# Optimization experiments

Measured on AMD Instinct MI355X. Metric: run time of the kernel, lower is better.

Reference implementation:

```python
import jax, jax.numpy as jnp
import numpy as np

KS = 3
K2 = KS * KS
PAD = 1


def conv2d(x, w, b=None, stride=1, pad=0):
    out = jax.lax.conv_general_dilated(
        x, w, (stride, stride), [(pad, pad), (pad, pad)],
        dimension_numbers=("NCHW", "OIHW", "NCHW"))
    if b is not None:
        out = out + b[None, :, None, None]
    return out


def setup_inputs() -> dict:
    key = jax.random.key(0)
    ks = jax.random.split(key, 11)
    B, C, H, W = 4, 64, 128, 128
    s = 0.05  # weight scale keeps offsets in a sane range
    return {
        "x":      jax.random.normal(ks[0], (B, C, H, W), jnp.float32),
        "ref":    jax.random.normal(ks[1], (B, C, H, W), jnp.float32),
        "w_cd":   jax.random.normal(ks[2], (C, 2 * C, 1, 1), jnp.float32) * s,
        "b_cd":   jax.random.normal(ks[3], (C,), jnp.float32) * s,
        "w_p":    jax.random.normal(ks[4], (2 * K2, C, 3, 3), jnp.float32) * s,
        "b_p":    jax.random.normal(ks[5], (2 * K2,), jnp.float32) * s,
        "w_m":    jax.random.normal(ks[6], (K2, C, 3, 3), jnp.float32) * s,
        "b_m":    jax.random.normal(ks[7], (K2,), jnp.float32) * s,
        "w_c":    jax.random.normal(ks[8], (K2 * C, C, 3, 3), jnp.float32) * s,
        "b_c":    jax.random.normal(ks[9], (K2 * C,), jnp.float32) * s,
        "w_conv": jax.random.normal(ks[10], (C, C, 3, 3), jnp.float32) * s,
    }


def _deform_forward(x, ref, w_cd, b_cd, w_p, b_p, w_m, b_m, w_c, b_c, w_conv):
    B, C, H, W = x.shape
    dt = x.dtype

    # offset / modulation / color nets on fused input
    fused = conv2d(jnp.concatenate([x, ref], axis=1), w_cd, b_cd)          # [B,C,H,W]
    off = conv2d(fused, w_p, b_p, pad=1)                                    # [B,2K2,H,W]
    mod = jax.nn.sigmoid(conv2d(fused, w_m, b_m, pad=1))                    # [B,K2,H,W]
    col = jnp.tanh(conv2d(fused, w_c, b_c, pad=1))                          # [B,K2*C,H,W]

    # zero-pad input; sampling grid carries the +padding shift (arange starts at 1)
    xp = jnp.pad(x, ((0, 0), (0, 0), (PAD, PAD), (PAD, PAD)))
    Hp, Wp = H + 2 * PAD, W + 2 * PAD

    gx = jnp.broadcast_to(jnp.arange(1, H + 1, dtype=dt)[:, None], (H, W))
    gy = jnp.broadcast_to(jnp.arange(1, W + 1, dtype=dt)[None, :], (H, W))
    r = (KS - 1) // 2
    cx, cy = jnp.meshgrid(jnp.arange(-r, r + 1, dtype=dt),
                          jnp.arange(-r, r + 1, dtype=dt), indexing="ij")
    px = gx[None, None] + off[:, :K2] + cx.ravel()[None, :, None, None]     # [B,K2,H,W]
    py = gy[None, None] + off[:, K2:] + cy.ravel()[None, :, None, None]

    # integer neighbors (detached, like torch .detach().floor())
    fx = jax.lax.stop_gradient(jnp.floor(px))
    fy = jax.lax.stop_gradient(jnp.floor(py))
    q_ltx = jnp.clip(fx, 0, Hp - 1); q_lty = jnp.clip(fy, 0, Wp - 1)
    q_rbx = jnp.clip(fx + 1, 0, Hp - 1); q_rby = jnp.clip(fy + 1, 0, Wp - 1)

    # clamped sampling locations for weights
    sx = jnp.clip(px, 0, Hp - 1)
    sy = jnp.clip(py, 0, Wp - 1)
    g_lt = (1 + (q_ltx - sx)) * (1 + (q_lty - sy))
    g_rb = (1 - (q_rbx - sx)) * (1 - (q_rby - sy))
    g_lb = (1 + (q_ltx - sx)) * (1 - (q_rby - sy))
    g_rt = (1 - (q_rbx - sx)) * (1 + (q_lty - sy))

    xf = xp.reshape(B, C, Hp * Wp)

    def gather(qx, qy):
        idx = (qx.astype(jnp.int32) * Wp + qy.astype(jnp.int32)).reshape(B, -1)
        out = jax.vmap(lambda m, i: m[:, i])(xf, idx)                       # [B,C,K2*H*W]
        return out.reshape(B, C, K2, H, W)

    pos = (g_lt[:, None] * gather(q_ltx, q_lty)
           + g_rb[:, None] * gather(q_rbx, q_rby)
           + g_lb[:, None] * gather(q_ltx, q_rby)
           + g_rt[:, None] * gather(q_rbx, q_lty))                          # [B,C,K2,H,W]

    inp = col.reshape(B, C, K2, H, W) + pos                                 # color deform
    inp = inp * mod[:, None]                                                # modulation

    # [B,C,kx,ky,H,W] -> [B,C,H,kx,W,ky] -> [B,C,H*ks,W*ks]
    io = inp.reshape(B, C, KS, KS, H, W).transpose(0, 1, 4, 2, 5, 3)
    io = io.reshape(B, C, H * KS, W * KS)
    return conv2d(io, w_conv, None, stride=KS)                              # [B,outc,H,W]


def reference(x, ref, w_cd, b_cd, w_p, b_p, w_m, b_m, w_c, b_c, w_conv):
    return _deform_forward(x, ref, w_cd, b_cd, w_p, b_p, w_m, b_m, w_c, b_c, w_conv)
```

## Files before the change

### kernel.cpp

```cpp
#include <hip/hip_runtime.h>
#include <hip/hip_bf16.h>
#include <math.h>

typedef short s16x8 __attribute__((ext_vector_type(8)));
typedef float f32x4 __attribute__((ext_vector_type(4)));

__device__ inline ushort f2bf(float f) {
  unsigned u = __float_as_uint(f);
  u = (u + 0x7FFF + ((u >> 16) & 1)) >> 16;
  return (ushort)u;
}
__device__ inline float bf2f(ushort u) {
  return __uint_as_float(((unsigned)u) << 16);
}
__device__ inline unsigned pkbf(float a, float b) {
  __hip_bfloat162 h = __float22bfloat162_rn(make_float2(a, b));
  return *(unsigned*)&h;
}
__device__ inline float fast_tanh(float v) {
  float e = __builtin_amdgcn_exp2f(v * 2.8853900817779268f);
  return 1.f - 2.f * __builtin_amdgcn_rcpf(e + 1.f);
}
__device__ inline float fast_sigmoid(float v) {
  float e = __builtin_amdgcn_exp2f(v * -1.4426950408889634f);
  return __builtin_amdgcn_rcpf(1.f + e);
}

__global__ __launch_bounds__(256) void k_fused(
    const float* __restrict__ x, const float* __restrict__ ref,
    const float* __restrict__ wcd, const float* __restrict__ bcd,
    const float* __restrict__ wp, const float* __restrict__ bp,
    const float* __restrict__ wm, const float* __restrict__ bm,
    const float* __restrict__ wc, const float* __restrict__ bc,
    const float* __restrict__ wconv,
    ushort* __restrict__ fusedt, ushort* __restrict__ xtb,
    ushort* __restrict__ Wpk, float* __restrict__ Bc, ushort* __restrict__ W2pk) {
  __shared__ float sxf[64][68];
  __shared__ __align__(16) ushort xt_lds[64 * 128];
  __shared__ float sb[64];

  if (blockIdx.x >= 1024) {
    int i = (blockIdx.x - 1024) * 256 + threadIdx.x;
    if (i < 368640) {
      int e = i & 7, lane = (i >> 3) & 63, mi = (i >> 9) & 3, ocq = (i >> 11) & 1;
      int hi = i >> 12;
      int ks = hi % 18, og = hi / 18;
      int g = og * 128 + ocq * 64 + mi * 16 + (lane & 15);
      int ci = ((ks & 1) << 5) + ((lane >> 4) << 3) + e;
      int kk = ks >> 1;
      int col = ci * 9 + kk;
      float v = 0.f;
      if (g < 18)       v = wp[g * 576 + col];
      else if (g < 27)  v = wm[(g - 18) * 576 + col];
      else if (g >= 64) {
        int j = g - 64;
        int cc = (j & 63) * 9 + (j >> 6);
        v = wc[cc * 576 + col];
      }
      Wpk[i] = f2bf(v);
    }
    if (i < 36864) {
      int e = i & 7, lane = (i >> 3) & 63, mi = (i >> 9) & 3, ks = i >> 11;
      int o = mi * 16 + (lane & 15);
      int p = (ks << 5) + ((lane >> 4) << 3) + e;
      int kk2 = p >> 6, c = p & 63;
      W2pk[i] = f2bf(wconv[o * 576 + c * 9 + kk2]);
    }
    if (i < 640) {
      float bv = 0.f;
      if (i < 18)       bv = bp[i];
      else if (i < 27)  bv = bm[i - 18];
      else if (i >= 64) {
        int j = i - 64;
        bv = bc[(j & 63) * 9 + (j >> 6)];
      }
      Bc[i] = bv;
    }
    return;
  }

  const int t = threadIdx.x;
  const int b = blockIdx.x >> 8, hw0 = (blockIdx.x & 255) << 6;
  if (t < 64) sb[t] = bcd[t];

  #pragma unroll
  for (int rep = 0; rep < 4; rep++) {
    int idx = t + (rep << 8);
    int ci = idx >> 4, p4 = (idx & 15) << 2;
    float4 v = *(const float4*)(x + ((size_t)((b << 6) + ci) << 14) + hw0 + p4);
    *(float4*)&sxf[ci][p4] = v;
  }
  __syncthreads();

  #pragma unroll
  for (int rep = 0; rep < 2; rep++) {
    int idx = t + (rep << 8);
    int px = idx >> 3, g = idx & 7;
    const int e0 = g << 3;
    uint4 ow;
    ow.x = pkbf(sxf[e0 + 0][px], sxf[e0 + 1][px]);
    ow.y = pkbf(sxf[e0 + 2][px], sxf[e0 + 3][px]);
    ow.z = pkbf(sxf[e0 + 4][px], sxf[e0 + 5][px]);
    ow.w = pkbf(sxf[e0 + 6][px], sxf[e0 + 7][px]);
    *(uint4*)(xt_lds + px * 128 + (((g + px) & 15) << 3)) = ow;
    *(uint4*)(xtb + (((size_t)b << 14) + hw0 + px) * 64 + (g << 3)) = ow;
  }
  __syncthreads();

  #pragma unroll
  for (int rep = 0; rep < 4; rep++) {
    int idx = t + (rep << 8);
    int ci = idx >> 4, p4 = (idx & 15) << 2;
    float4 v = *(const float4*)(ref + ((size_t)((b << 6) + ci) << 14) + hw0 + p4);
    *(float4*)&sxf[ci][p4] = v;
  }
  __syncthreads();

  #pragma unroll
  for (int rep = 0; rep < 2; rep++) {
    int idx = t + (rep << 8);
    int px = idx >> 3, g = (idx & 7) + 8;
    const int e0 = (g & 7) << 3;
    uint4 ow;
    ow.x = pkbf(sxf[e0 + 0][px], sxf[e0 + 1][px]);
    ow.y = pkbf(sxf[e0 + 2][px], sxf[e0 + 3][px]);
    ow.z = pkbf(sxf[e0 + 4][px], sxf[e0 + 5][px]);
    ow.w = pkbf(sxf[e0 + 6][px], sxf[e0 + 7][px]);
    *(uint4*)(xt_lds + px * 128 + (((g + px) & 15) << 3)) = ow;
  }
  __syncthreads();

  const int lane = t & 63, wv4 = t >> 6;
  const int ocl = lane & 15, kb = lane >> 4;
  const int ocr = (wv4 << 4) + ocl;
  f32x4 acc[4];
  #pragma unroll
  for (int ni = 0; ni < 4; ni++) acc[ni] = (f32x4){0.f, 0.f, 0.f, 0.f};
  #pragma unroll
  for (int s = 0; s < 4; s++) {
    const int gA = (s << 2) + kb;
    const float4* wr4 = (const float4*)(wcd + ocr * 128 + (gA << 3));
    float4 wa = wr4[0], wb2 = wr4[1];
    unsigned aw[4];
    aw[0] = pkbf(wa.x, wa.y);   aw[1] = pkbf(wa.z, wa.w);
    aw[2] = pkbf(wb2.x, wb2.y); aw[3] = pkbf(wb2.z, wb2.w);
    s16x8 af = *(const s16x8*)aw;
    #pragma unroll
    for (int ni = 0; ni < 4; ni++) {
      const int px = (ni << 4) + ocl;
      s16x8 bf8 = *(const s16x8*)(xt_lds + px * 128 + (((gA + px) & 15) << 3));
      acc[ni] = __builtin_amdgcn_mfma_f32_16x16x32_bf16(af, bf8, acc[ni], 0, 0, 0);
    }
  }
  const float4 b4 = *(const float4*)&sb[(wv4 << 4) + (kb << 2)];
  #pragma unroll
  for (int ni = 0; ni < 4; ni++) {
    const int px = (ni << 4) + ocl;
    uint2 o;
    o.x = pkbf(acc[ni][0] + b4.x, acc[ni][1] + b4.y);
    o.y = pkbf(acc[ni][2] + b4.z, acc[ni][3] + b4.w);
    *(uint2*)(fusedt + (((size_t)(b << 14) + hw0 + px) << 6) + (wv4 << 4) + (kb << 2)) = o;
  }
}

__global__ __launch_bounds__(256) void k_all(
    const ushort* __restrict__ Wpk, const ushort* __restrict__ fusedt,
    const float* __restrict__ Bc, const ushort* __restrict__ xtb,
    const ushort* __restrict__ W2pk, float* __restrict__ out) {
  __shared__ __align__(16) ushort sF[3 * 66 * 64];
  __shared__ __align__(16) ushort colT[64 * 64];
  __shared__ float homT[64 * 27];
  const int t = threadIdx.x;
  const int lane = t & 63, wv = t >> 6;
  const int rowid = blockIdx.x;
  const int b = rowid >> 8;
  const int rem = rowid & 255;
  const int h = rem >> 1, hf = rem & 1;
  const int w0 = hf << 6;
  const int hw0 = (h << 7) + w0;

  for (int idx = t; idx < 1584; idx += 256) {
    int p = idx >> 3, j = idx & 7;
    int row = p / 66, w1 = p - row * 66;
    int gh = h + row - 1, gw = w0 + w1 - 1;
    uint4 v = make_uint4(0u, 0u, 0u, 0u);
    if (gh >= 0 && gh < 128 && (unsigned)gw < 128u)
      v = *(const uint4*)(fusedt + ((size_t)((b << 14) + (gh << 7) + gw) << 6) + j * 8);
    int slot = (j + w1) & 7;
    *(uint4*)(sF + (p << 6) + slot * 8) = v;
  }
  __syncthreads();

  const int pxq = wv & 1, rowq = wv >> 1;
  const int nif = lane & 15, kb = lane >> 4, quad = lane >> 4;

  if (rowq == 0) {
    f32x4 acc[2][2];
    #pragma unroll
    for (int mi = 0; mi < 2; mi++)
      #pragma unroll
      for (int ni = 0; ni < 2; ni++) acc[mi][ni] = (f32x4){0.f, 0.f, 0.f, 0.f};
    __builtin_amdgcn_s_setprio(1);
    #pragma unroll 2
    for (int ks = 0; ks < 18; ks++) {
      const int kk = ks >> 1, half = ks & 1;
      const int dr = kk / 3, dc = kk - dr * 3;
      const ushort* wp8 = Wpk + ((size_t)(ks << 12)) + (lane << 3);
      s16x8 af[2], bfr[2];
      #pragma unroll
      for (int mi = 0; mi < 2; mi++)
        af[mi] = *(const s16x8*)(wp8 + (mi << 9));
      const int gci = half * 4 + kb;
      #pragma unroll
      for (int ni = 0; ni < 2; ni++) {
        int r = (pxq << 5) + ni * 16 + nif;
        int w1 = r + dc;
        int slot = (gci + w1) & 7;
        bfr[ni] = *(const s16x8*)(sF + ((dr * 66 + w1) << 6) + slot * 8);
      }
      #pragma unroll
      for (int mi = 0; mi < 2; mi++)
        #pragma unroll
        for (int ni = 0; ni < 2; ni++)
          acc[mi][ni] = __builtin_amdgcn_mfma_f32_16x16x32_bf16(af[mi], bfr[ni], acc[mi][ni], 0, 0, 0);
    }
    __builtin_amdgcn_s_setprio(0);
    #pragma unroll
    for (int mi = 0; mi < 2; mi++) {
      #pragma unroll
      for (int ni = 0; ni < 2; ni++) {
        int px = (pxq << 5) + ni * 16 + nif;
        #pragma unroll
        for (int r = 0; r < 4; r++) {
          int g = mi * 16 + (quad << 2) + r;
          float v = acc[mi][ni][r] + Bc[g];
          if (g < 18)       homT[px * 27 + g] = v;
          else if (g < 27)  homT[px * 27 + g] = fast_sigmoid(v);
        }
      }
    }
  }

  const int cq = t >> 6, pxl = t & 63, c0 = cq << 4;
  const int ww = w0 + pxl;
  const ushort* xb = xtb + ((size_t)b << 20);

  f32x4 aco[2][2];
  #pragma unroll
  for (int mi = 0; mi < 2; mi++)
    #pragma unroll
    for (int ni = 0; ni < 2; ni++) aco[mi][ni] = (f32x4){0.f, 0.f, 0.f, 0.f};

  #pragma unroll 1
  for (int k = 0; k < 9; k++) {
    const int q = 1 + k, og = q >> 1, ocq = q & 1;
    f32x4 acc[2][2];
    #pragma unroll
    for (int mi = 0; mi < 2; mi++)
      #pragma unroll
      for (int ni = 0; ni < 2; ni++) acc[mi][ni] = (f32x4){0.f, 0.f, 0.f, 0.f};
    __builtin_amdgcn_s_setprio(1);
    #pragma unroll 2
    for (int ks = 0; ks < 18; ks++) {
      const int kk = ks >> 1, half = ks & 1;
      const int dr = kk / 3, dc = kk - dr * 3;
      const ushort* wp8 = Wpk + ((size_t)((((og * 18 + ks) << 1) + ocq) << 11)) + (lane << 3);
      s16x8 af[2], bfr[2];
      #pragma unroll
      for (int mi = 0; mi < 2; mi++)
        af[mi] = *(const s16x8*)(wp8 + (((rowq << 1) + mi) << 9));
      const int gci = half * 4 + kb;
      #pragma unroll
      for (int ni = 0; ni < 2; ni++) {
        int r = (pxq << 5) + ni * 16 + nif;
        int w1 = r + dc;
        int slot = (gci + w1) & 7;
        bfr[ni] = *(const s16x8*)(sF + ((dr * 66 + w1) << 6) + slot * 8);
      }
      #pragma unroll
      for (int mi = 0; mi < 2; mi++)
        #pragma unroll
        for (int ni = 0; ni < 2; ni++)
          acc[mi][ni] = __builtin_amdgcn_mfma_f32_16x16x32_bf16(af[mi], bfr[ni], acc[mi][ni], 0, 0, 0);
    }
    __builtin_amdgcn_s_setprio(0);
    __syncthreads();

    #pragma unroll
    for (int mi = 0; mi < 2; mi++) {
      #pragma unroll
      for (int ni = 0; ni < 2; ni++) {
        int px = (pxq << 5) + ni * 16 + nif;
        int c = (rowq << 5) + mi * 16 + (quad << 2);
        float4 b4 = *(const float4*)(Bc + 64 + (k << 6) + c);
        ushort v4[4];
        v4[0] = f2bf(fast_tanh(acc[mi][ni][0] + b4.x));
        v4[1] = f2bf(fast_tanh(acc[mi][ni][1] + b4.y));
        v4[2] = f2bf(fast_tanh(acc[mi][ni][2] + b4.z));
        v4[3] = f2bf(fast_tanh(acc[mi][ni][3] + b4.w));
        int slot = ((c >> 3) + px) & 7;
        *(uint2*)(colT + (px << 6) + slot * 8 + (c & 7)) = *(uint2*)v4;
      }
    }
    __syncthreads();

    {
      float ox = homT[pxl * 27 + k];
      float oy = homT[pxl * 27 + 9 + k];
      float mk = homT[pxl * 27 + 18 + k];
      float px_ = (float)(h + k / 3) + ox;
      float py_ = (float)(ww + k % 3) + oy;
      float fx = floorf(px_), fy = floorf(py_);
      float qltx = fminf(fmaxf(fx, 0.f), 129.f);
      float qlty = fminf(fmaxf(fy, 0.f), 129.f);
      float qrbx = fminf(fmaxf(fx + 1.f, 0.f), 129.f);
      float qrby = fminf(fmaxf(fy + 1.f, 0.f), 129.f);
      float sx = fminf(fmaxf(px_, 0.f), 129.f);
      float sy = fminf(fmaxf(py_, 0.f), 129.f);
      float ax = 1.f + qltx - sx, bx = 1.f - qrbx + sx;
      float ay = 1.f + qlty - sy, by = 1.f - qrby + sy;
      int iltx = (int)qltx, ilty = (int)qlty, irbx = (int)qrbx, irby = (int)qrby;
      bool vltx = (iltx >= 1) && (iltx <= 128);
      bool vlty = (ilty >= 1) && (ilty <= 128);
      bool vrbx = (irbx >= 1) && (irbx <= 128);
      bool vrby = (irby >= 1) && (irby <= 128);
      float wl[4];
      int   ofs[4];
      wl[0] = (vltx && vlty) ? ax * ay : 0.f;
      wl[1] = (vrbx && vrby) ? bx * by : 0.f;
      wl[2] = (vltx && vrby) ? ax * by : 0.f;
      wl[3] = (vrbx && vlty) ? bx * ay : 0.f;
      ofs[0] = (vltx && vlty) ? ((iltx - 1) << 7) + (ilty - 1) : 0;
      ofs[1] = (vrbx && vrby) ? ((irbx - 1) << 7) + (irby - 1) : 0;
      ofs[2] = (vltx && vrby) ? ((iltx - 1) << 7) + (irby - 1) : 0;
      ofs[3] = (vrbx && vlty) ? ((irbx - 1) << 7) + (ilty - 1) : 0;

      float pos[16];
      #pragma unroll
      for (int j = 0; j < 16; j++) pos[j] = 0.f;
      #pragma unroll
      for (int corner = 0; corner < 4; corner++) {
        const ushort* p = xb + ((size_t)ofs[corner] << 6) + c0;
        float wgt = wl[corner];
        ushort tmp[16];
        *(uint4*)(tmp)     = *(const uint4*)(p);
        *(uint4*)(tmp + 8) = *(const uint4*)(p + 8);
        #pragma unroll
        for (int j = 0; j < 16; j++) pos[j] += wgt * bf2f(tmp[j]);
      }
      #pragma unroll
      for (int q2 = 0; q2 < 2; q2++) {
        int chunk = (cq << 1) + q2;
        int slot = (chunk + pxl) & 7;
        ushort* cp = colT + (pxl << 6) + slot * 8;
        ushort ct[8];
        *(uint4*)ct = *(const uint4*)cp;
        #pragma unroll
        for (int j = 0; j < 8; j++)
          ct[j] = f2bf((bf2f(ct[j]) + pos[q2 * 8 + j]) * mk);
        *(uint4*)cp = *(uint4*)ct;
      }
    }
    __syncthreads();

    __builtin_amdgcn_s_setprio(1);
    #pragma unroll
    for (int khalf = 0; khalf < 2; khalf++) {
      int ks2 = (k << 1) + khalf;
      s16x8 af[2], bfr[2];
      #pragma unroll
      for (int mi = 0; mi < 2; mi++)
        af[mi] = *(const s16x8*)(W2pk + ((((ks2 << 2) + (rowq << 1) + mi) << 6) + lane) * 8);
      const int g0 = (khalf << 2) + kb;
      #pragma unroll
      for (int ni = 0; ni < 2; ni++) {
        int r = (pxq << 5) + ni * 16 + nif;
        int slot = (g0 + r) & 7;
        bfr[ni] = *(const s16x8*)(colT + (r << 6) + slot * 8);
      }
      #pragma unroll
      for (int mi = 0; mi < 2; mi++)
        #pragma unroll
        for (int ni = 0; ni < 2; ni++)
          aco[mi][ni] = __builtin_amdgcn_mfma_f32_16x16x32_bf16(af[mi], bfr[ni], aco[mi][ni], 0, 0, 0);
    }
    __builtin_amdgcn_s_setprio(0);
  }

  #pragma unroll
  for (int mi = 0; mi < 2; mi++) {
    #pragma unroll
    for (int ni = 0; ni < 2; ni++) {
      int hwp = hw0 + (pxq << 5) + ni * 16 + nif;
      #pragma unroll
      for (int r = 0; r < 4; r++) {
        int o = (rowq << 5) + mi * 16 + (quad << 2) + r;
        out[(((size_t)b * 64 + o) << 14) + hwp] = aco[mi][ni][r];
      }
    }
  }
}

extern "C" void kernel_launch(void* const* d_in, const int* in_sizes, int n_in,
                              void* d_out, int out_size, void* d_ws, size_t ws_size,
                              hipStream_t stream) {
  const float* x     = (const float*)d_in[0];
  const float* ref   = (const float*)d_in[1];
  const float* wcd   = (const float*)d_in[2];
  const float* bcd   = (const float*)d_in[3];
  const float* wp    = (const float*)d_in[4];
  const float* bp    = (const float*)d_in[5];
  const float* wm    = (const float*)d_in[6];
  const float* bm    = (const float*)d_in[7];
  const float* wc    = (const float*)d_in[8];
  const float* bc    = (const float*)d_in[9];
  const float* wconv = (const float*)d_in[10];
  float* out = (float*)d_out;

  char* w8 = (char*)d_ws;
  ushort* Wpk     = (ushort*)(w8 + 0);
  float*  Bc      = (float*)(w8 + 737280);
  ushort* W2pk    = (ushort*)(w8 + 739840);
  ushort* fusedt  = (ushort*)(w8 + 813568);
  ushort* xtb     = (ushort*)(w8 + 9202176);

  k_fused <<<2464, 256, 0, stream>>>(x, ref, wcd, bcd, wp, bp, wm, bm, wc, bc, wconv,
                                     fusedt, xtb, Wpk, Bc, W2pk);
  k_all   <<<1024, 256, 0, stream>>>(Wpk, fusedt, Bc, xtb, W2pk, out);
}
```

Baseline: 198.2 us.

## Load NCHW input directly into transposed bf16 LDS and fold weight packing into conv blocks

The first kernel no longer stages x and ref through an fp32 shared tile with four barriers. Each thread now reads 8 channel-strided scalars per pixel, packs them to bf16 and writes them straight into the swizzled LDS tile, with a single barrier. The transposed x copy is written out from LDS afterwards. Weight and bias packing moves from 1440 dedicated extra blocks into a grid-stride tail of the 1024 conv blocks, and launch bounds request 8 blocks per CU. Dropping the fp32 tile frees LDS for occupancy, at the cost of less vectorized strided global loads.

```diff
diff --git a/kernel.cpp b/kernel.cpp
--- a/kernel.cpp
+++ b/kernel.cpp
@@ -26,7 +26,7 @@
   return __builtin_amdgcn_rcpf(1.f + e);
 }
 
-__global__ __launch_bounds__(256) void k_fused(
+__global__ __launch_bounds__(256, 8) void k_fused(
     const float* __restrict__ x, const float* __restrict__ ref,
     const float* __restrict__ wcd, const float* __restrict__ bcd,
     const float* __restrict__ wp, const float* __restrict__ bp,
@@ -35,100 +35,44 @@
     const float* __restrict__ wconv,
     ushort* __restrict__ fusedt, ushort* __restrict__ xtb,
     ushort* __restrict__ Wpk, float* __restrict__ Bc, ushort* __restrict__ W2pk) {
-  __shared__ float sxf[64][68];
   __shared__ __align__(16) ushort xt_lds[64 * 128];
   __shared__ float sb[64];
-
-  if (blockIdx.x >= 1024) {
-    int i = (blockIdx.x - 1024) * 256 + threadIdx.x;
-    if (i < 368640) {
-      int e = i & 7, lane = (i >> 3) & 63, mi = (i >> 9) & 3, ocq = (i >> 11) & 1;
-      int hi = i >> 12;
-      int ks = hi % 18, og = hi / 18;
-      int g = og * 128 + ocq * 64 + mi * 16 + (lane & 15);
-      int ci = ((ks & 1) << 5) + ((lane >> 4) << 3) + e;
-      int kk = ks >> 1;
-      int col = ci * 9 + kk;
-      float v = 0.f;
-      if (g < 18)       v = wp[g * 576 + col];
-      else if (g < 27)  v = wm[(g - 18) * 576 + col];
-      else if (g >= 64) {
-        int j = g - 64;
-        int cc = (j & 63) * 9 + (j >> 6);
-        v = wc[cc * 576 + col];
-      }
-      Wpk[i] = f2bf(v);
-    }
-    if (i < 36864) {
-      int e = i & 7, lane = (i >> 3) & 63, mi = (i >> 9) & 3, ks = i >> 11;
-      int o = mi * 16 + (lane & 15);
-      int p = (ks << 5) + ((lane >> 4) << 3) + e;
-      int kk2 = p >> 6, c = p & 63;
-      W2pk[i] = f2bf(wconv[o * 576 + c * 9 + kk2]);
-    }
-    if (i < 640) {
-      float bv = 0.f;
-      if (i < 18)       bv = bp[i];
-      else if (i < 27)  bv = bm[i - 18];
-      else if (i >= 64) {
-        int j = i - 64;
-        bv = bc[(j & 63) * 9 + (j >> 6)];
-      }
-      Bc[i] = bv;
-    }
-    return;
-  }
 
   const int t = threadIdx.x;
   const int b = blockIdx.x >> 8, hw0 = (blockIdx.x & 255) << 6;
   if (t < 64) sb[t] = bcd[t];
 
   #pragma unroll
-  for (int rep = 0; rep < 4; rep++) {
-    int idx = t + (rep << 8);
-    int ci = idx >> 4, p4 = (idx & 15) << 2;
-    float4 v = *(const float4*)(x + ((size_t)((b << 6) + ci) << 14) + hw0 + p4);
-    *(float4*)&sxf[ci][p4] = v;
+  for (int rep = 0; rep < 2; rep++) {
+    const int px = t & 63;
+    const int g = (t >> 6) + (rep << 2);
+    const float* xrow = x   + ((size_t)((b << 6) + (g << 3)) << 14) + hw0 + px;
+    const float* rrow = ref + ((size_t)((b << 6) + (g << 3)) << 14) + hw0 + px;
+    float v[8];
+    #pragma unroll
+    for (int e = 0; e < 8; e++) v[e] = xrow[(size_t)e << 14];
+    uint4 ow;
+    ow.x = pkbf(v[0], v[1]); ow.y = pkbf(v[2], v[3]);
+    ow.z = pkbf(v[4], v[5]); ow.w = pkbf(v[6], v[7]);
+    *(uint4*)(xt_lds + px * 128 + (((g + px) & 15) << 3)) = ow;
+    #pragma unroll
+    for (int e = 0; e < 8; e++) v[e] = rrow[(size_t)e << 14];
+    uint4 orf;
+    orf.x = pkbf(v[0], v[1]); orf.y = pkbf(v[2], v[3]);
+    orf.z = pkbf(v[4], v[5]); orf.w = pkbf(v[6], v[7]);
+    *(uint4*)(xt_lds + px * 128 + (((g + 8 + px) & 15) << 3)) = orf;
   }
   __syncthreads();
 
-  #pragma unroll
-  for (int rep = 0; rep < 2; rep++) {
-    int idx = t + (rep << 8);
-    int px = idx >> 3, g = idx & 7;
-    const int e0 = g << 3;
-    uint4 ow;
-    ow.x = pkbf(sxf[e0 + 0][px], sxf[e0 + 1][px]);
-    ow.y = pkbf(sxf[e0 + 2][px], sxf[e0 + 3][px]);
-    ow.z = pkbf(sxf[e0 + 4][px], sxf[e0 + 5][px]);
-    ow.w = pkbf(sxf[e0 + 6][px], sxf[e0 + 7][px]);
-    *(uint4*)(xt_lds + px * 128 + (((g + px) & 15) << 3)) = ow;
-    *(uint4*)(xtb + (((size_t)b << 14) + hw0 + px) * 64 + (g << 3)) = ow;
-  }
-  __syncthreads();
-
-  #pragma unroll
-  for (int rep = 0; rep < 4; rep++) {
-    int idx = t + (rep << 8);
-    int ci = idx >> 4, p4 = (idx & 15) << 2;
-    float4 v = *(const float4*)(ref + ((size_t)((b << 6) + ci) << 14) + hw0 + p4);
-    *(float4*)&sxf[ci][p4] = v;
-  }
-  __syncthreads();
-
-  #pragma unroll
-  for (int rep = 0; rep < 2; rep++) {
-    int idx = t + (rep << 8);
-    int px = idx >> 3, g = (idx & 7) + 8;
-    const int e0 = (g & 7) << 3;
-    uint4 ow;
-    ow.x = pkbf(sxf[e0 + 0][px], sxf[e0 + 1][px]);
-    ow.y = pkbf(sxf[e0 + 2][px], sxf[e0 + 3][px]);
-    ow.z = pkbf(sxf[e0 + 4][px], sxf[e0 + 5][px]);
-    ow.w = pkbf(sxf[e0 + 6][px], sxf[e0 + 7][px]);
-    *(uint4*)(xt_lds + px * 128 + (((g + px) & 15) << 3)) = ow;
-  }
-  __syncthreads();
+  {
+    const int px = t >> 2, j0 = (t & 3) << 1;
+    const ushort* rowp = xt_lds + px * 128;
+    uint4 c0 = *(const uint4*)(rowp + (((j0 + px) & 15) << 3));
+    uint4 c1 = *(const uint4*)(rowp + (((j0 + 1 + px) & 15) << 3));
+    ushort* dst = xtb + (((size_t)b << 14) + hw0 + px) * 64 + (j0 << 3);
+    *(uint4*)dst       = c0;
+    *(uint4*)(dst + 8) = c1;
+  }
 
   const int lane = t & 63, wv4 = t >> 6;
   const int ocl = lane & 15, kb = lane >> 4;
@@ -160,6 +104,43 @@
     o.x = pkbf(acc[ni][0] + b4.x, acc[ni][1] + b4.y);
     o.y = pkbf(acc[ni][2] + b4.z, acc[ni][3] + b4.w);
     *(uint2*)(fusedt + (((size_t)(b << 14) + hw0 + px) << 6) + (wv4 << 4) + (kb << 2)) = o;
+  }
+
+  const int gid = blockIdx.x * 256 + t;
+  for (int i = gid; i < 368640; i += 262144) {
+    int e = i & 7, lne = (i >> 3) & 63, mi = (i >> 9) & 3, ocq = (i >> 11) & 1;
+    int hi = i >> 12;
+    int ks = hi % 18, og = hi / 18;
+    int g = og * 128 + ocq * 64 + mi * 16 + (lne & 15);
+    int ci = ((ks & 1) << 5) + ((lne >> 4) << 3) + e;
+    int kk = ks >> 1;
+    int col = ci * 9 + kk;
+    float v = 0.f;
+    if (g < 18)       v = wp[g * 576 + col];
+    else if (g < 27)  v = wm[(g - 18) * 576 + col];
+    else if (g >= 64) {
+      int j = g - 64;
+      int cc = (j & 63) * 9 + (j >> 6);
+      v = wc[cc * 576 + col];
+    }
+    Wpk[i] = f2bf(v);
+  }
+  if (gid < 36864) {
+    int e = gid & 7, lne = (gid >> 3) & 63, mi = (gid >> 9) & 3, ks = gid >> 11;
+    int o = mi * 16 + (lne & 15);
+    int p = (ks << 5) + ((lne >> 4) << 3) + e;
+    int kk2 = p >> 6, c = p & 63;
+    W2pk[gid] = f2bf(wconv[o * 576 + c * 9 + kk2]);
+  }
+  if (gid < 640) {
+    float bv = 0.f;
+    if (gid < 18)       bv = bp[gid];
+    else if (gid < 27)  bv = bm[gid - 18];
+    else if (gid >= 64) {
+      int j = gid - 64;
+      bv = bc[(j & 63) * 9 + (j >> 6)];
+    }
+    Bc[gid] = bv;
   }
 }
 
@@ -424,7 +405,7 @@
   ushort* fusedt  = (ushort*)(w8 + 813568);
   ushort* xtb     = (ushort*)(w8 + 9202176);
 
-  k_fused <<<2464, 256, 0, stream>>>(x, ref, wcd, bcd, wp, bp, wm, bm, wc, bc, wconv,
+  k_fused <<<1024, 256, 0, stream>>>(x, ref, wcd, bcd, wp, bp, wm, bm, wc, bc, wconv,
                                      fusedt, xtb, Wpk, Bc, W2pk);
   k_all   <<<1024, 256, 0, stream>>>(Wpk, fusedt, Bc, xtb, W2pk, out);
 }
```

Result: no change. 197.5 us (-0.3%).
